# Performance work log

Measured on AMD Instinct MI355X. Metric: run time of the kernel, lower is better.

The kernel has to match this reference:

```python
import jax, jax.numpy as jnp
import numpy as np

HEAD_SIZE = 64
NEG_INF = float('-inf')


def setup_inputs() -> dict:
    key = jax.random.key(0)
    ks = jax.random.split(key, 4)
    B, S, H, D = 8, 4096, 1024, HEAD_SIZE
    scale = 1.0 / np.sqrt(H)
    return {
        'x': jax.random.normal(ks[0], (B, S, H), dtype=jnp.float32),
        'Wq': jax.random.normal(ks[1], (H, D), dtype=jnp.float32) * scale,
        'bq': jnp.zeros((D,), dtype=jnp.float32),
        'Wk': jax.random.normal(ks[2], (H, D), dtype=jnp.float32) * scale,
        'bk': jnp.zeros((D,), dtype=jnp.float32),
        'Wv': jax.random.normal(ks[3], (H, D), dtype=jnp.float32) * scale,
        'bv': jnp.zeros((D,), dtype=jnp.float32),
    }


def reference(x, Wq, bq, Wk, bk, Wv, bv):
    # x: [B, S, H]; projections -> [B, S, D]
    B, S, H = x.shape
    q = jnp.einsum('bsh,hd->bsd', x, Wq) + bq
    k = jnp.einsum('bsh,hd->bsd', x, Wk) + bk
    v = jnp.einsum('bsh,hd->bsd', x, Wv) + bv
    # raw scores [B, S, S]
    scores = jnp.einsum('bqd,bkd->bqk', q, k)
    # causal mask applied BEFORE scaling (matches original; -inf/scale == -inf)
    causal = jnp.tril(jnp.ones((S, S), dtype=bool))
    scores = jnp.where(causal, scores, NEG_INF)
    scale = 1.0 / jnp.sqrt(jnp.asarray(q.shape[-1], dtype=scores.dtype))
    attn = jax.nn.softmax(scores * scale, axis=-1)
    # dropout = 0.0 (eval) -> identity
    return jnp.einsum('bqk,bkd->bqd', attn, v)
```

## Files before the change

### kernel.cpp

```cpp
#include <hip/hip_runtime.h>
#include <hip/hip_bf16.h>
#include <math.h>

#define SEQ 4096
#define HID 1024
#define DH  64
#define NB  8
#define QSCALE 0.18033688011112042f

typedef unsigned short ushort_t;
typedef unsigned int   uint_t;
typedef __attribute__((ext_vector_type(8)))  short  bf16x8;
typedef __attribute__((ext_vector_type(4)))  float  f32x4;
typedef __attribute__((ext_vector_type(16))) float  f32x16;
typedef __attribute__((ext_vector_type(4)))  uint_t u32x4;
typedef __attribute__((ext_vector_type(2)))  uint_t u32x2;

static __device__ __forceinline__ ushort_t f2bf(float f) {
    __hip_bfloat16 h = __float2bfloat16(f);
    return *reinterpret_cast<ushort_t*>(&h);
}
static __device__ __forceinline__ ushort_t f2bf_fast(float f) {
    uint_t u = __float_as_uint(f);
    return (ushort_t)((u + 0x8000u) >> 16);
}
static __device__ __forceinline__ uint_t bfpair(float lo, float hi) {
    return (uint_t)f2bf_fast(lo) | ((uint_t)f2bf_fast(hi) << 16);
}

static __device__ __forceinline__ void gld_lds16(const void* g, void* s) {
    __builtin_amdgcn_global_load_lds(
        (const __attribute__((address_space(1))) void*)g,
        (__attribute__((address_space(3))) void*)s, 16, 0, 0);
}

__global__ __launch_bounds__(256) void prep_w(
    const float* __restrict__ Wq, const float* __restrict__ Wk,
    const float* __restrict__ Wv, ushort_t* __restrict__ wts)
{
    __shared__ ushort_t tr[64][72];
    const int bx   = blockIdx.x;
    const int mmat = bx >> 4;
    const int kt   = bx & 15;
    const float* W  = (mmat == 0) ? Wq : (mmat == 1) ? Wk : Wv;
    const float  sc = (mmat == 0) ? QSCALE : 1.0f;

    const int t  = threadIdx.x;
    const int kr = t >> 2, kc = (t & 3) * 16;
    const float* src = W + (size_t)(kt * 64 + kr) * DH + kc;
    float4 a0 = *(const float4*)(src);
    float4 a1 = *(const float4*)(src + 4);
    float4 a2 = *(const float4*)(src + 8);
    float4 a3 = *(const float4*)(src + 12);
    float vv[16] = {a0.x,a0.y,a0.z,a0.w, a1.x,a1.y,a1.z,a1.w,
                    a2.x,a2.y,a2.z,a2.w, a3.x,a3.y,a3.z,a3.w};
    #pragma unroll
    for (int i = 0; i < 16; ++i) tr[kr][kc + i] = f2bf(vv[i] * sc);
    __syncthreads();

    const int cl = t >> 2, jc = (t & 3) * 16;
    const int c  = mmat * 64 + cl;
    ushort_t* dst = wts + kt * 12288 + c * 64;
    #pragma unroll
    for (int jj = 0; jj < 16; ++jj) {
        int j = jc + jj;
        dst[((j >> 3) ^ (cl & 7)) * 8 + (j & 7)] = tr[j][cl];
    }
}

__global__ __launch_bounds__(256) void qkv_proj(
    const float* __restrict__ x, const ushort_t* __restrict__ wts,
    const float* __restrict__ bq, const float* __restrict__ bk,
    const float* __restrict__ bv,
    ushort_t* __restrict__ qimg, ushort_t* __restrict__ kimg,
    ushort_t* __restrict__ vimg)
{
    __shared__ ushort_t bw[2][12288];

    const int t  = threadIdx.x;
    const int w  = t >> 6, l = t & 63, lr = l & 15, g = l >> 4;
    const int row0 = blockIdx.x * 64;
    const int row  = row0 + w * 16 + lr;
    const int ch0 = (g ^ (lr & 7)) * 8;
    const int ch1 = ((g + 4) ^ (lr & 7)) * 8;

    f32x4 acc[12];
    #pragma unroll
    for (int i = 0; i < 12; ++i) acc[i] = (f32x4){0.f,0.f,0.f,0.f};

    const char* wbase = (const char*)wts;
    const int   wlo   = w * 1024 + l * 16;
    const float* xrow = x + (size_t)row * HID + g * 8;

    float4 Xa0, Xa1, Xb0, Xb1;
    {
        Xa0 = *(const float4*)(xrow);
        Xa1 = *(const float4*)(xrow + 4);
        Xb0 = *(const float4*)(xrow + 32);
        Xb1 = *(const float4*)(xrow + 36);
        char* bdst = (char*)&bw[0][0] + w * 1024;
        #pragma unroll
        for (int i = 0; i < 6; ++i)
            gld_lds16(wbase + wlo + i * 4096, bdst + i * 4096);
    }

    for (int kt = 0; kt < 16; ++kt) {
        const int buf = kt & 1;
        float4 Na0, Na1, Nb0, Nb1;
        if (kt < 15) {
            char* bdst = (char*)&bw[buf ^ 1][0] + w * 1024;
            const char* bsrc = wbase + (size_t)(kt + 1) * 24576 + wlo;
            #pragma unroll
            for (int i = 0; i < 6; ++i)
                gld_lds16(bsrc + i * 4096, bdst + i * 4096);
            const float* xn = xrow + (kt + 1) * 64;
            Na0 = *(const float4*)(xn);
            Na1 = *(const float4*)(xn + 4);
            Nb0 = *(const float4*)(xn + 32);
            Nb1 = *(const float4*)(xn + 36);
        }
        if (kt < 15) asm volatile("s_waitcnt vmcnt(10)" ::: "memory");
        else         asm volatile("s_waitcnt vmcnt(0)"  ::: "memory");
        __builtin_amdgcn_s_barrier();
        asm volatile("" ::: "memory");

        bf16x8 af0, af1;
        {
            u32x4 p;
            p.x = bfpair(Xa0.x, Xa0.y); p.y = bfpair(Xa0.z, Xa0.w);
            p.z = bfpair(Xa1.x, Xa1.y); p.w = bfpair(Xa1.z, Xa1.w);
            af0 = *(bf16x8*)&p;
            u32x4 q;
            q.x = bfpair(Xb0.x, Xb0.y); q.y = bfpair(Xb0.z, Xb0.w);
            q.z = bfpair(Xb1.x, Xb1.y); q.w = bfpair(Xb1.z, Xb1.w);
            af1 = *(bf16x8*)&q;
        }
        #pragma unroll
        for (int ct = 0; ct < 12; ++ct) {
            const int c = ct * 16 + lr;
            bf16x8 b0 = *(bf16x8*)&bw[buf][c * 64 + ch0];
            bf16x8 b1 = *(bf16x8*)&bw[buf][c * 64 + ch1];
            acc[ct] = __builtin_amdgcn_mfma_f32_16x16x32_bf16(af0, b0, acc[ct], 0, 0, 0);
            acc[ct] = __builtin_amdgcn_mfma_f32_16x16x32_bf16(af1, b1, acc[ct], 0, 0, 0);
        }
        asm volatile("" ::: "memory");
        __builtin_amdgcn_s_barrier();
        Xa0 = Na0; Xa1 = Na1; Xb0 = Nb0; Xb1 = Nb1;
    }

    #pragma unroll
    for (int ct = 0; ct < 12; ++ct) {
        const int c    = ct * 16 + lr;
        const int mmat = c >> 6;
        const int cc   = c & 63;
        const float* bp = (mmat == 0) ? bq : (mmat == 1) ? bk : bv;
        const float bias = bp[cc] * (mmat == 0 ? QSCALE : 1.0f);
        #pragma unroll
        for (int r = 0; r < 4; ++r) {
            const int s = row0 + w * 16 + g * 4 + r;
            const ushort_t v = f2bf_fast(acc[ct][r] + bias);
            if (mmat == 0)
                qimg[(size_t)s * 64 + cc] = v;
            else if (mmat == 1)
                kimg[(size_t)(s >> 6) * 4096 + (s & 63) * 64 +
                     ((cc >> 3) ^ (s & 7)) * 8 + (cc & 7)] = v;
            else
                vimg[(size_t)(s >> 6) * 4096 + (size_t)cc * 64 +
                     (((s & 63) >> 3) ^ (cc & 7)) * 8 + (s & 7)] = v;
        }
    }
}

__global__ __launch_bounds__(256) void attn(
    const ushort_t* __restrict__ qimg, const ushort_t* __restrict__ kimg,
    const ushort_t* __restrict__ vimg,
    float* __restrict__ Opart, float* __restrict__ Lpart)
{
    __shared__ ushort_t kvs[3][8192];
    float* const oscp  = (float*)&kvs[0][0];
    float* const lredp = (float*)&kvs[1][0];

    const int t  = threadIdx.x;
    const int w  = t >> 6, l = t & 63, lw = l & 31, hs = l >> 5;
    const int qh = w & 1;
    const int kh = w >> 1;
    const int bx   = blockIdx.x;
    const int half = bx & 1;
    const int u    = bx >> 1;
    const int qt   = 63 - (u >> 3);
    const int b    = u & 7;
    const int q0   = qt * 64;
    const int n    = qt + 1, hn = n >> 1;
    const int t0   = half ? hn : 0;
    const int t1   = half ? n : hn;
    const int qq   = q0 + qh * 32 + lw;

    bf16x8 qf[4];
    {
        const ushort_t* qp = qimg + (size_t)(b * SEQ + qq) * 64 + hs * 8;
        #pragma unroll
        for (int ks = 0; ks < 4; ++ks) qf[ks] = *(const bf16x8*)(qp + ks * 16);
    }

    f32x16 o0, o1;
    #pragma unroll
    for (int r = 0; r < 16; ++r) { o0[r] = 0.f; o1[r] = 0.f; }
    float lpart = 0.f;

    const char* kbase = (const char*)kimg + (size_t)b * 524288;
    const char* vbase = (const char*)vimg + (size_t)b * 524288;
    const int wo = w * 1024;
    const int lo = l * 16;

    auto STAGE = [&](int ss, int tt) {
        const char* ks = kbase + (size_t)tt * 8192;
        const char* vs = vbase + (size_t)tt * 8192;
        char* lk = (char*)&kvs[ss][0];
        gld_lds16(ks + wo + lo,        lk + wo);
        gld_lds16(ks + wo + lo + 4096, lk + wo + 4096);
        gld_lds16(vs + wo + lo,        lk + wo + 8192);
        gld_lds16(vs + wo + lo + 4096, lk + wo + 12288);
    };

    if (t0     < t1) STAGE(0, t0);
    if (t0 + 1 < t1) STAGE(1, t0 + 1);

    int cur = 0;
    for (int kt = t0; kt < t1; ++kt) {
        const int sd = (cur == 0) ? 2 : cur - 1;
        if (kt + 2 < t1) STAGE(sd, kt + 2);
        if      (kt + 2 < t1) asm volatile("s_waitcnt vmcnt(8)" ::: "memory");
        else if (kt + 1 < t1) asm volatile("s_waitcnt vmcnt(4)" ::: "memory");
        else                  asm volatile("s_waitcnt vmcnt(0)" ::: "memory");
        __builtin_amdgcn_s_barrier();
        asm volatile("" ::: "memory");

        const ushort_t* kb   = &kvs[cur][0];
        const int       krow = kh * 32 + lw;
        const ushort_t* krb  = kb + krow * 64;
        f32x16 s;
        #pragma unroll
        for (int r = 0; r < 16; ++r) s[r] = 0.f;
        #pragma unroll
        for (int ks = 0; ks < 4; ++ks) {
            bf16x8 kf = *(const bf16x8*)(krb + (((ks * 2 + hs) ^ (krow & 7)) * 8));
            s = __builtin_amdgcn_mfma_f32_32x32x16_bf16(kf, qf[ks], s, 0, 0, 0);
        }

        float p[16];
        if (kt == qt) {
            #pragma unroll
            for (int r = 0; r < 16; ++r) {
                const int kvg = kt * 64 + kh * 32 + (r & 3) + 8 * (r >> 2) + 4 * hs;
                p[r] = (kvg > qq) ? 0.f : __builtin_amdgcn_exp2f(s[r]);
            }
        } else {
            #pragma unroll
            for (int r = 0; r < 16; ++r) p[r] = __builtin_amdgcn_exp2f(s[r]);
        }
        {
            float s0 = (p[0] + p[1])  + (p[2] + p[3]);
            float s1 = (p[4] + p[5])  + (p[6] + p[7]);
            float s2 = (p[8] + p[9])  + (p[10] + p[11]);
            float s3 = (p[12] + p[13]) + (p[14] + p[15]);
            lpart += (s0 + s1) + (s2 + s3);
        }

        const ushort_t* vb = &kvs[cur][4096];
        #pragma unroll
        for (int ks2 = 0; ks2 < 2; ++ks2) {
            uint_t a0 = bfpair(p[ks2*8 + 0], p[ks2*8 + 1]);
            uint_t b0 = bfpair(p[ks2*8 + 4], p[ks2*8 + 5]);
            uint_t a1 = bfpair(p[ks2*8 + 2], p[ks2*8 + 3]);
            uint_t b1 = bfpair(p[ks2*8 + 6], p[ks2*8 + 7]);
            asm("v_permlane32_swap_b32 %0, %1" : "+v"(a0), "+v"(b0));
            asm("v_permlane32_swap_b32 %0, %1" : "+v"(a1), "+v"(b1));
            u32x4 pw = { a0, a1, b0, b1 };
            bf16x8 paf = *(bf16x8*)&pw;
            const int sl8 = kh * 4 + ks2 * 2 + hs;
            {
                const int vr0 = lw;
                bf16x8 vf0 = *(const bf16x8*)(vb + vr0 * 64 + ((sl8 ^ (vr0 & 7)) * 8));
                o0 = __builtin_amdgcn_mfma_f32_32x32x16_bf16(paf, vf0, o0, 0, 0, 0);
                const int vr1 = 32 + lw;
                bf16x8 vf1 = *(const bf16x8*)(vb + vr1 * 64 + ((sl8 ^ (vr1 & 7)) * 8));
                o1 = __builtin_amdgcn_mfma_f32_32x32x16_bf16(paf, vf1, o1, 0, 0, 0);
            }
        }
        asm volatile("" ::: "memory");
        __builtin_amdgcn_s_barrier();
        cur = (cur == 2) ? 0 : cur + 1;
    }

    if (kh == 1) {
        const int lbase = (qh * 64 + l) * 32;
        #pragma unroll
        for (int i = 0; i < 4; ++i) {
            f32x4 v = { o0[4*i], o0[4*i+1], o0[4*i+2], o0[4*i+3] };
            *(f32x4*)&oscp[lbase + ((i ^ (l & 7)) * 4)] = v;
        }
        #pragma unroll
        for (int i = 0; i < 4; ++i) {
            f32x4 v = { o1[4*i], o1[4*i+1], o1[4*i+2], o1[4*i+3] };
            *(f32x4*)&oscp[lbase + (((i + 4) ^ (l & 7)) * 4)] = v;
        }
        float lsum = lpart + __shfl_xor(lpart, 32);
        if (hs == 0) lredp[qh * 32 + lw] = lsum;
    }
    __syncthreads();
    if (kh == 0) {
        const int lbase = (qh * 64 + l) * 32;
        #pragma unroll
        for (int i = 0; i < 4; ++i) {
            f32x4 v = *(const f32x4*)&oscp[lbase + ((i ^ (l & 7)) * 4)];
            o0[4*i] += v.x; o0[4*i+1] += v.y; o0[4*i+2] += v.z; o0[4*i+3] += v.w;
        }
        #pragma unroll
        for (int i = 0; i < 4; ++i) {
            f32x4 v = *(const f32x4*)&oscp[lbase + (((i + 4) ^ (l & 7)) * 4)];
            o1[4*i] += v.x; o1[4*i+1] += v.y; o1[4*i+2] += v.z; o1[4*i+3] += v.w;
        }
        const float lt = (lpart + __shfl_xor(lpart, 32)) + lredp[qh * 32 + lw];

        const int m = b * 64 + qt;
        float* Op = Opart + ((size_t)half * 512 + m) * 4096;
        #pragma unroll
        for (int r = 0; r < 16; ++r) {
            const int qrow = qh * 32 + (r & 3) + 8 * (r >> 2) + 4 * hs;
            Op[qrow * 64 + lw]      = o0[r];
            Op[qrow * 64 + 32 + lw] = o1[r];
        }
        if (hs == 0)
            Lpart[((size_t)half * 512 + m) * 64 + qh * 32 + lw] = lt;
    }
}

__global__ __launch_bounds__(256) void merge_o(
    const float* __restrict__ Opart, const float* __restrict__ Lpart,
    float* __restrict__ outg)
{
    const int m = blockIdx.x;
    const int b = m >> 6, qt = m & 63;
    const int t = threadIdx.x;
    const int row = t >> 2, c = (t & 3) * 16;

    const float* A = Opart + (size_t)m * 4096 + row * 64 + c;
    const float* B = Opart + (size_t)(512 + m) * 4096 + row * 64 + c;
    const float la = Lpart[(size_t)m * 64 + row];
    const float lb = Lpart[(size_t)(512 + m) * 64 + row];
    const float inv = 1.0f / (la + lb);
    float* dst = outg + ((size_t)b * SEQ + qt * 64 + row) * 64 + c;
    #pragma unroll
    for (int j = 0; j < 4; ++j) {
        float4 va = *(const float4*)(A + j * 4);
        float4 vb = *(const float4*)(B + j * 4);
        float4 vo = { (va.x + vb.x) * inv, (va.y + vb.y) * inv,
                      (va.z + vb.z) * inv, (va.w + vb.w) * inv };
        *(float4*)(dst + j * 4) = vo;
    }
}

extern "C" void kernel_launch(void* const* d_in, const int* in_sizes, int n_in,
                              void* d_out, int out_size, void* d_ws, size_t ws_size,
                              hipStream_t stream) {
    const float* x  = (const float*)d_in[0];
    const float* Wq = (const float*)d_in[1];
    const float* bq = (const float*)d_in[2];
    const float* Wk = (const float*)d_in[3];
    const float* bk = (const float*)d_in[4];
    const float* Wv = (const float*)d_in[5];
    const float* bv = (const float*)d_in[6];
    float* out = (float*)d_out;

    const size_t per = (size_t)NB * SEQ * DH;
    ushort_t* q   = (ushort_t*)d_ws;
    ushort_t* k   = q + per;
    ushort_t* v   = k + per;
    ushort_t* wts = v + per;
    float* Opart  = (float*)((char*)d_ws + (size_t)(16u << 20));
    float* Lpart  = (float*)((char*)d_ws + (size_t)(40u << 20));

    prep_w  <<<dim3(48),   256, 0, stream>>>(Wq, Wk, Wv, wts);
    qkv_proj<<<dim3(512),  256, 0, stream>>>(x, wts, bq, bk, bv, q, k, v);
    attn    <<<dim3(1024), 256, 0, stream>>>(q, k, v, Opart, Lpart);
    merge_o <<<dim3(512),  256, 0, stream>>>(Opart, Lpart, out);
}
```

Before: 252.0 us.

## Enlarge QKV projection tiles to 128 rows with 32x32 MFMA and triple-buffered weights

The QKV projection now computes 128 rows per block using 32x32x16 MFMAs, so each staged weight tile is reused across twice as many rows. It also moves from double to triple buffering in dynamic LDS, with prefetch issued after the barrier so the trailing barrier can be dropped. The attention loop likewise moves staging after the barrier and removes its per-iteration trailing barrier. The cost is larger LDS use and fewer blocks (256 instead of 512), which may lower occupancy and leave some CUs idle.

```diff
diff --git a/kernel.cpp b/kernel.cpp
--- a/kernel.cpp
+++ b/kernel.cpp
@@ -75,89 +75,95 @@
     ushort_t* __restrict__ qimg, ushort_t* __restrict__ kimg,
     ushort_t* __restrict__ vimg)
 {
-    __shared__ ushort_t bw[2][12288];
+    extern __shared__ char dynls[];
 
     const int t  = threadIdx.x;
-    const int w  = t >> 6, l = t & 63, lr = l & 15, g = l >> 4;
-    const int row0 = blockIdx.x * 64;
-    const int row  = row0 + w * 16 + lr;
-    const int ch0 = (g ^ (lr & 7)) * 8;
-    const int ch1 = ((g + 4) ^ (lr & 7)) * 8;
-
-    f32x4 acc[12];
-    #pragma unroll
-    for (int i = 0; i < 12; ++i) acc[i] = (f32x4){0.f,0.f,0.f,0.f};
+    const int w  = t >> 6, l = t & 63, lw = l & 31, hs = l >> 5;
+    const int row0 = blockIdx.x * 128;
+    const int row  = row0 + w * 32 + lw;
+
+    f32x16 acc[6];
+    #pragma unroll
+    for (int i = 0; i < 6; ++i)
+        for (int r = 0; r < 16; ++r) acc[i][r] = 0.f;
 
     const char* wbase = (const char*)wts;
     const int   wlo   = w * 1024 + l * 16;
-    const float* xrow = x + (size_t)row * HID + g * 8;
-
-    float4 Xa0, Xa1, Xb0, Xb1;
-    {
-        Xa0 = *(const float4*)(xrow);
-        Xa1 = *(const float4*)(xrow + 4);
-        Xb0 = *(const float4*)(xrow + 32);
-        Xb1 = *(const float4*)(xrow + 36);
-        char* bdst = (char*)&bw[0][0] + w * 1024;
+    const float* xrow = x + (size_t)row * HID + hs * 8;
+
+    auto STAGEW = [&](int ss, int tile) {
+        char* bdst = dynls + ss * 24576 + w * 1024;
+        const char* bsrc = wbase + (size_t)tile * 24576 + wlo;
         #pragma unroll
         for (int i = 0; i < 6; ++i)
-            gld_lds16(wbase + wlo + i * 4096, bdst + i * 4096);
-    }
-
+            gld_lds16(bsrc + i * 4096, bdst + i * 4096);
+    };
+
+    float4 Xc[4][2], Xn[4][2];
+
+    STAGEW(0, 0);
+    #pragma unroll
+    for (int ks = 0; ks < 4; ++ks) {
+        Xc[ks][0] = *(const float4*)(xrow + ks * 16);
+        Xc[ks][1] = *(const float4*)(xrow + ks * 16 + 4);
+    }
+    STAGEW(1, 1);
+
+    int cs = 0;
     for (int kt = 0; kt < 16; ++kt) {
-        const int buf = kt & 1;
-        float4 Na0, Na1, Nb0, Nb1;
-        if (kt < 15) {
-            char* bdst = (char*)&bw[buf ^ 1][0] + w * 1024;
-            const char* bsrc = wbase + (size_t)(kt + 1) * 24576 + wlo;
-            #pragma unroll
-            for (int i = 0; i < 6; ++i)
-                gld_lds16(bsrc + i * 4096, bdst + i * 4096);
-            const float* xn = xrow + (kt + 1) * 64;
-            Na0 = *(const float4*)(xn);
-            Na1 = *(const float4*)(xn + 4);
-            Nb0 = *(const float4*)(xn + 32);
-            Nb1 = *(const float4*)(xn + 36);
-        }
-        if (kt < 15) asm volatile("s_waitcnt vmcnt(10)" ::: "memory");
-        else         asm volatile("s_waitcnt vmcnt(0)"  ::: "memory");
+        if (kt < 15) asm volatile("s_waitcnt vmcnt(6)" ::: "memory");
+        else         asm volatile("s_waitcnt vmcnt(0)" ::: "memory");
         __builtin_amdgcn_s_barrier();
         asm volatile("" ::: "memory");
 
-        bf16x8 af0, af1;
-        {
+        if (kt < 15) {
+            const float* xn = xrow + (kt + 1) * 64;
+            #pragma unroll
+            for (int ks = 0; ks < 4; ++ks) {
+                Xn[ks][0] = *(const float4*)(xn + ks * 16);
+                Xn[ks][1] = *(const float4*)(xn + ks * 16 + 4);
+            }
+        }
+        if (kt < 14) {
+            const int sd = (cs == 0) ? 2 : cs - 1;
+            STAGEW(sd, kt + 2);
+        }
+
+        bf16x8 af[4];
+        #pragma unroll
+        for (int ks = 0; ks < 4; ++ks) {
             u32x4 p;
-            p.x = bfpair(Xa0.x, Xa0.y); p.y = bfpair(Xa0.z, Xa0.w);
-            p.z = bfpair(Xa1.x, Xa1.y); p.w = bfpair(Xa1.z, Xa1.w);
-            af0 = *(bf16x8*)&p;
-            u32x4 q;
-            q.x = bfpair(Xb0.x, Xb0.y); q.y = bfpair(Xb0.z, Xb0.w);
-            q.z = bfpair(Xb1.x, Xb1.y); q.w = bfpair(Xb1.z, Xb1.w);
-            af1 = *(bf16x8*)&q;
-        }
-        #pragma unroll
-        for (int ct = 0; ct < 12; ++ct) {
-            const int c = ct * 16 + lr;
-            bf16x8 b0 = *(bf16x8*)&bw[buf][c * 64 + ch0];
-            bf16x8 b1 = *(bf16x8*)&bw[buf][c * 64 + ch1];
-            acc[ct] = __builtin_amdgcn_mfma_f32_16x16x32_bf16(af0, b0, acc[ct], 0, 0, 0);
-            acc[ct] = __builtin_amdgcn_mfma_f32_16x16x32_bf16(af1, b1, acc[ct], 0, 0, 0);
-        }
-        asm volatile("" ::: "memory");
-        __builtin_amdgcn_s_barrier();
-        Xa0 = Na0; Xa1 = Na1; Xb0 = Nb0; Xb1 = Nb1;
-    }
-
-    #pragma unroll
-    for (int ct = 0; ct < 12; ++ct) {
-        const int c    = ct * 16 + lr;
-        const int mmat = c >> 6;
-        const int cc   = c & 63;
-        const float* bp = (mmat == 0) ? bq : (mmat == 1) ? bk : bv;
-        const float bias = bp[cc] * (mmat == 0 ? QSCALE : 1.0f);
-        #pragma unroll
-        for (int r = 0; r < 4; ++r) {
-            const int s = row0 + w * 16 + g * 4 + r;
+            p.x = bfpair(Xc[ks][0].x, Xc[ks][0].y);
+            p.y = bfpair(Xc[ks][0].z, Xc[ks][0].w);
+            p.z = bfpair(Xc[ks][1].x, Xc[ks][1].y);
+            p.w = bfpair(Xc[ks][1].z, Xc[ks][1].w);
+            af[ks] = *(bf16x8*)&p;
+        }
+        const ushort_t* bwS = (const ushort_t*)(dynls + cs * 24576);
+        #pragma unroll
+        for (int ct = 0; ct < 6; ++ct) {
+            const ushort_t* bp = bwS + (ct * 32 + lw) * 64;
+            #pragma unroll
+            for (int ks = 0; ks < 4; ++ks) {
+                bf16x8 bf = *(const bf16x8*)(bp + (((ks * 2 + hs) ^ (lw & 7)) * 8));
+                acc[ct] = __builtin_amdgcn_mfma_f32_32x32x16_bf16(af[ks], bf, acc[ct], 0, 0, 0);
+            }
+        }
+        #pragma unroll
+        for (int ks = 0; ks < 4; ++ks) { Xc[ks][0] = Xn[ks][0]; Xc[ks][1] = Xn[ks][1]; }
+        cs = (cs == 2) ? 0 : cs + 1;
+    }
+
+    const int rowbase = row0 + w * 32;
+    #pragma unroll
+    for (int ct = 0; ct < 6; ++ct) {
+        const int mmat = ct >> 1;
+        const int cc   = ((ct & 1) << 5) | lw;
+        const float* bpv = (mmat == 0) ? bq : (mmat == 1) ? bk : bv;
+        const float bias = bpv[cc] * (mmat == 0 ? QSCALE : 1.0f);
+        #pragma unroll
+        for (int r = 0; r < 16; ++r) {
+            const int s = rowbase + (r & 3) + 8 * (r >> 2) + 4 * hs;
             const ushort_t v = f2bf_fast(acc[ct][r] + bias);
             if (mmat == 0)
                 qimg[(size_t)s * 64 + cc] = v;
@@ -227,13 +233,14 @@
 
     int cur = 0;
     for (int kt = t0; kt < t1; ++kt) {
-        const int sd = (cur == 0) ? 2 : cur - 1;
-        if (kt + 2 < t1) STAGE(sd, kt + 2);
-        if      (kt + 2 < t1) asm volatile("s_waitcnt vmcnt(8)" ::: "memory");
-        else if (kt + 1 < t1) asm volatile("s_waitcnt vmcnt(4)" ::: "memory");
-        else                  asm volatile("s_waitcnt vmcnt(0)" ::: "memory");
+        if (kt + 1 < t1) asm volatile("s_waitcnt vmcnt(4)" ::: "memory");
+        else             asm volatile("s_waitcnt vmcnt(0)" ::: "memory");
         __builtin_amdgcn_s_barrier();
         asm volatile("" ::: "memory");
+        if (kt + 2 < t1) {
+            const int sd = (cur == 0) ? 2 : cur - 1;
+            STAGE(sd, kt + 2);
+        }
 
         const ushort_t* kb   = &kvs[cur][0];
         const int       krow = kh * 32 + lw;
@@ -287,10 +294,9 @@
                 o1 = __builtin_amdgcn_mfma_f32_32x32x16_bf16(paf, vf1, o1, 0, 0, 0);
             }
         }
-        asm volatile("" ::: "memory");
-        __builtin_amdgcn_s_barrier();
         cur = (cur == 2) ? 0 : cur + 1;
     }
+    __syncthreads();
 
     if (kh == 1) {
         const int lbase = (qh * 64 + l) * 32;
@@ -380,8 +386,8 @@
     float* Opart  = (float*)((char*)d_ws + (size_t)(16u << 20));
     float* Lpart  = (float*)((char*)d_ws + (size_t)(40u << 20));
 
-    prep_w  <<<dim3(48),   256, 0, stream>>>(Wq, Wk, Wv, wts);
-    qkv_proj<<<dim3(512),  256, 0, stream>>>(x, wts, bq, bk, bv, q, k, v);
-    attn    <<<dim3(1024), 256, 0, stream>>>(q, k, v, Opart, Lpart);
-    merge_o <<<dim3(512),  256, 0, stream>>>(Opart, Lpart, out);
-}
+    prep_w  <<<dim3(48),   256, 0,     stream>>>(Wq, Wk, Wv, wts);
+    qkv_proj<<<dim3(256),  256, 73728, stream>>>(x, wts, bq, bk, bv, q, k, v);
+    attn    <<<dim3(1024), 256, 0,     stream>>>(q, k, v, Opart, Lpart);
+    merge_o <<<dim3(512),  256, 0,     stream>>>(Opart, Lpart, out);
+}
```

New measurement: 261.3 us. 3.7% more time.
